# Performance work log

Measured on AMD Instinct MI355X. Metric: run time of the kernel, lower is better.

## Reference

```python
import jax, jax.numpy as jnp
import numpy as np

TOP_K = 2

def setup_inputs() -> dict:
    key = jax.random.key(0)
    ks = jax.random.split(key, 5)
    N, D, E, H, O = 2048, 1024, 16, 2048, 1024
    s_in = 1.0 / np.sqrt(D)
    s_h = 1.0 / np.sqrt(H)
    return {
        "z": jax.random.normal(ks[0], (N, D), dtype=jnp.float32),
        "router_w": jax.random.normal(ks[1], (E, D), dtype=jnp.float32) * s_in,
        "router_b": jnp.zeros((E,), dtype=jnp.float32),
        "w1": jax.random.normal(ks[2], (E, H, D), dtype=jnp.float32) * s_in,
        "b1": jnp.zeros((E, H), dtype=jnp.float32),
        "w2": jax.random.normal(ks[3], (E, O, H), dtype=jnp.float32) * s_h,
        "b2": jnp.zeros((E, O), dtype=jnp.float32),
    }

def reference(z, router_w, router_b, w1, b1, w2, b2):
    # Router: softmax over experts, then top-k with renormalized weights
    logits = z @ router_w.T + router_b                      # [N, E]
    probs = jax.nn.softmax(logits, axis=-1)                 # [N, E]
    topk_prob, topk_idx = jax.lax.top_k(probs, TOP_K)       # [N, K]
    topk_prob = topk_prob / topk_prob.sum(axis=-1, keepdims=True)

    # Dense all-expert MLP (faithful to original mix(): every expert on every token)
    h = jax.nn.gelu(jnp.einsum('nd,ehd->neh', z, w1) + b1, approximate=False)  # [N, E, H]
    expert_out = jnp.einsum('neh,eoh->neo', h, w2) + b2                        # [N, E, O]

    # Gather top-k expert outputs and combine with routing weights
    picked = jnp.take_along_axis(expert_out, topk_idx[:, :, None], axis=1)     # [N, K, O]
    return (picked * topk_prob[:, :, None]).sum(axis=1)                        # [N, O]
```

## Files before the change

### kernel.cpp

```cpp
#include <hip/hip_runtime.h>
#include <hip/hip_bf16.h>
#include <math.h>

#define N_TOK 2048
#define DIM   1024
#define NE    16
#define NH    2048
#define NO    1024

typedef __attribute__((ext_vector_type(8))) short short8;
typedef __attribute__((ext_vector_type(4))) float f32x4;

__device__ __forceinline__ unsigned short f2bf(float f) {
  union { float f; unsigned u; } v; v.f = f;
  unsigned r = v.u + 0x7FFFu + ((v.u >> 16) & 1u);
  return (unsigned short)(r >> 16);
}

__device__ __forceinline__ short8 pack8(float4 a, float4 b) {
  short8 r;
  r[0] = (short)f2bf(a.x); r[1] = (short)f2bf(a.y);
  r[2] = (short)f2bf(a.z); r[3] = (short)f2bf(a.w);
  r[4] = (short)f2bf(b.x); r[5] = (short)f2bf(b.y);
  r[6] = (short)f2bf(b.z); r[7] = (short)f2bf(b.w);
  return r;
}

__device__ __forceinline__ unsigned pkbf(float x, float y) {
  float2 f; f.x = x; f.y = y;
  __hip_bfloat162 b = __float22bfloat162_rn(f);
  unsigned u; __builtin_memcpy(&u, &b, 4);
  return u;
}
__device__ __forceinline__ short8 cvt8(float4 a, float4 b) {
  union { short8 s; unsigned u[4]; } r;
  r.u[0] = pkbf(a.x, a.y); r.u[1] = pkbf(a.z, a.w);
  r.u[2] = pkbf(b.x, b.y); r.u[3] = pkbf(b.z, b.w);
  return r.s;
}

__device__ __forceinline__ void glds16(const void* g, void* l) {
  __builtin_amdgcn_global_load_lds(
      (const __attribute__((address_space(1))) void*)g,
      (__attribute__((address_space(3))) void*)l, 16, 0, 0);
}

__global__ __launch_bounds__(256) void router_kernel(
    const float* __restrict__ z, const float* __restrict__ rw,
    const float* __restrict__ rb, int* __restrict__ counts,
    int* __restrict__ list, float* __restrict__ tkw) {
  const int n = blockIdx.x;
  const int t = threadIdx.x;
  const int e = t >> 4, sub = t & 15;
  const float* zr = z + (size_t)n * DIM;
  const float* wr = rw + (size_t)e * DIM;
  double acc = 0.0;
#pragma unroll
  for (int i = 0; i < 16; ++i) {
    const int d = i * 64 + sub * 4;
    const float4 zv = *(const float4*)(zr + d);
    const float4 wv = *(const float4*)(wr + d);
    acc += (double)zv.x * wv.x + (double)zv.y * wv.y
         + (double)zv.z * wv.z + (double)zv.w * wv.w;
  }
  acc += __shfl_xor(acc, 8, 16);
  acc += __shfl_xor(acc, 4, 16);
  acc += __shfl_xor(acc, 2, 16);
  acc += __shfl_xor(acc, 1, 16);
  __shared__ double logits[NE];
  if (sub == 0) logits[e] = acc + (double)rb[e];
  __syncthreads();
  if (t == 0) {
    int i0 = -1, i1 = -1; double v0 = -1e300, v1 = -1e300;
    for (int i = 0; i < NE; ++i) {
      const double v = logits[i];
      if (v > v0) { v1 = v0; i1 = i0; v0 = v; i0 = i; }
      else if (v > v1) { v1 = v; i1 = i; }
    }
    const double w0 = 1.0 / (1.0 + exp(v1 - v0));
    tkw[n * 2 + 0] = (float)w0;
    tkw[n * 2 + 1] = (float)(1.0 - w0);
    const int p0 = atomicAdd(&counts[i0], 1); list[i0 * N_TOK + p0] = n * 2;
    const int p1 = atomicAdd(&counts[i1], 1); list[i1 * N_TOK + p1] = n * 2 + 1;
  }
}

__global__ __launch_bounds__(256) void convert_z_kernel(
    const float* __restrict__ z, unsigned short* __restrict__ zbf) {
  const int i = (blockIdx.x * 256 + threadIdx.x) * 8;
  const float4 a = *(const float4*)(z + i);
  const float4 b = *(const float4*)(z + i + 4);
  *(short8*)(zbf + i) = pack8(a, b);
}

#define BM 128
#define BN 128
#define BK 64
#define NNT1 (NH / BN)
#define NNT2 (NO / BN)
#define MT_LEVELS 8
#define NT1 (DIM / BK)
#define NT2 (NH / BK)
#define ASZ (BM * BK * 2)
#define BSZ (BN * BK * 2)

__device__ __forceinline__ void decode_bid(int bid, int nent, int& mt, int& ent) {
  if (bid < 2 * nent) {
    mt = (bid >> 3) & 1;
    ent = (bid >> 4) * 8 + (bid & 7);
  } else {
    const int t2 = bid - 2 * nent;
    mt = 2 + t2 / nent;
    ent = t2 - (mt - 2) * nent;
  }
}

__global__ __launch_bounds__(256, 2) void gemm1_kernel(
    const unsigned short* __restrict__ zbf, const float* __restrict__ w1,
    const float* __restrict__ b1, const int* __restrict__ counts,
    const int* __restrict__ list, unsigned short* __restrict__ h) {
  int mt, ent;
  decode_bid(blockIdx.x, NE * NNT1, mt, ent);
  const int e  = ent >> 4;
  const int nt = ent & 15;
  const int ne = counts[e];
  if (mt * BM >= ne) return;
  const int t = threadIdx.x;

  __shared__ __align__(16) unsigned char As[2 * ASZ];
  __shared__ __align__(16) unsigned char Bs[2 * BSZ];
  __shared__ int ent_s[BM];
  if (t < BM) {
    const int idx = mt * BM + t;
    ent_s[t] = (idx < ne) ? list[e * N_TOK + idx] : -1;
  }
  __syncthreads();

  const int lane = t & 63, w = t >> 6;
  const unsigned short* aP[4];
  unsigned char* aL[4];
  {
    const int l3 = lane >> 3, c7 = lane & 7;
#pragma unroll
    for (int p = 0; p < 4; ++p) {
      const int CI = w + 4 * p;
      const int R = 8 * CI + l3;
      const int c = c7 ^ (R & 7);
      const int en = ent_s[R];
      aP[p] = zbf + (size_t)(en >= 0 ? (en >> 1) : 0) * DIM + c * 8;
      aL[p] = As + CI * 1024;
    }
  }
  const int bR = w * 32 + (lane >> 1);
  const int bh = lane & 1;
  const float* bSrc = w1 + ((size_t)e * NH + (size_t)(nt * BN + bR)) * DIM + bh * 32;
  unsigned char* bW[4];
#pragma unroll
  for (int j = 0; j < 4; ++j)
    bW[j] = Bs + bR * 128 + (((bh * 4 + j) ^ (bR & 7)) << 4);

  const int wm = (w & 1) * 64, wn = (w >> 1) * 64;
  const int l15 = lane & 15, quad = lane >> 4;

  f32x4 acc[4][4];
#pragma unroll
  for (int i = 0; i < 4; ++i)
#pragma unroll
    for (int j = 0; j < 4; ++j) acc[i][j] = (f32x4){0.f, 0.f, 0.f, 0.f};

  float4 breg[8];
#pragma unroll
  for (int p = 0; p < 4; ++p) glds16(aP[p], aL[p]);
#pragma unroll
  for (int j = 0; j < 8; ++j) breg[j] = *(const float4*)(bSrc + j * 4);
#pragma unroll
  for (int j = 0; j < 4; ++j)
    *(short8*)(bW[j]) = cvt8(breg[2 * j], breg[2 * j + 1]);
  __syncthreads();

  for (int kt = 0; kt < NT1; ++kt) {
    const int cur = kt & 1, nxt = cur ^ 1;
    const int k1 = (kt + 1) * BK;
    if (kt + 1 < NT1) {
#pragma unroll
      for (int p = 0; p < 4; ++p) glds16(aP[p] + k1, aL[p] + nxt * ASZ);
#pragma unroll
      for (int j = 0; j < 8; ++j) breg[j] = *(const float4*)(bSrc + k1 + j * 4);
    }
    const unsigned char* Ac = As + cur * ASZ;
    const unsigned char* Bc = Bs + cur * BSZ;
#pragma unroll
    for (int kk = 0; kk < BK; kk += 32) {
      short8 af[4], bfr[4];
      const int c0 = (kk >> 3) + quad;
#pragma unroll
      for (int i = 0; i < 4; ++i) {
        const int R = wm + i * 16 + l15;
        af[i] = *(const short8*)(Ac + R * 128 + ((c0 ^ (R & 7)) << 4));
      }
#pragma unroll
      for (int j = 0; j < 4; ++j) {
        const int R = wn + j * 16 + l15;
        bfr[j] = *(const short8*)(Bc + R * 128 + ((c0 ^ (R & 7)) << 4));
      }
#pragma unroll
      for (int i = 0; i < 4; ++i)
#pragma unroll
        for (int j = 0; j < 4; ++j)
          acc[i][j] = __builtin_amdgcn_mfma_f32_16x16x32_bf16(af[i], bfr[j], acc[i][j], 0, 0, 0);
    }
    if (kt + 1 < NT1) {
#pragma unroll
      for (int j = 0; j < 4; ++j)
        *(short8*)(bW[j] + nxt * BSZ) = cvt8(breg[2 * j], breg[2 * j + 1]);
      __syncthreads();
    }
  }

  const int r4 = quad * 4;
#pragma unroll
  for (int i = 0; i < 4; ++i) {
#pragma unroll
    for (int reg = 0; reg < 4; ++reg) {
      const int row = wm + i * 16 + r4 + reg;
      const int en = ent_s[row];
      if (en < 0) continue;
      unsigned short* hrow = h + (size_t)en * NH;
#pragma unroll
      for (int j = 0; j < 4; ++j) {
        const int col = nt * BN + wn + j * 16 + l15;
        float v = acc[i][j][reg] + b1[e * NH + col];
        v = 0.5f * v * (1.0f + erff(v * 0.70710678118654752f));
        hrow[col] = f2bf(v);
      }
    }
  }
}

__global__ __launch_bounds__(256, 2) void gemm2_kernel(
    const unsigned short* __restrict__ h, const float* __restrict__ w2,
    const float* __restrict__ b2, const int* __restrict__ counts,
    const int* __restrict__ list, float* __restrict__ contrib) {
  int mt, ent;
  decode_bid(blockIdx.x, NE * NNT2, mt, ent);
  const int e  = ent >> 3;
  const int nt = ent & 7;
  const int ne = counts[e];
  if (mt * BM >= ne) return;
  const int t = threadIdx.x;

  __shared__ __align__(16) unsigned char As[2 * ASZ];
  __shared__ __align__(16) unsigned char Bs[2 * BSZ];
  __shared__ int ent_s[BM];
  if (t < BM) {
    const int idx = mt * BM + t;
    ent_s[t] = (idx < ne) ? list[e * N_TOK + idx] : -1;
  }
  __syncthreads();

  const int lane = t & 63, w = t >> 6;
  const unsigned short* aP[4];
  unsigned char* aL[4];
  {
    const int l3 = lane >> 3, c7 = lane & 7;
#pragma unroll
    for (int p = 0; p < 4; ++p) {
      const int CI = w + 4 * p;
      const int R = 8 * CI + l3;
      const int c = c7 ^ (R & 7);
      const int en = ent_s[R];
      aP[p] = h + (size_t)(en >= 0 ? en : 0) * NH + c * 8;
      aL[p] = As + CI * 1024;
    }
  }
  const int bR = w * 32 + (lane >> 1);
  const int bh = lane & 1;
  const float* bSrc = w2 + ((size_t)e * NO + (size_t)(nt * BN + bR)) * NH + bh * 32;
  unsigned char* bW[4];
#pragma unroll
  for (int j = 0; j < 4; ++j)
    bW[j] = Bs + bR * 128 + (((bh * 4 + j) ^ (bR & 7)) << 4);

  const int wm = (w & 1) * 64, wn = (w >> 1) * 64;
  const int l15 = lane & 15, quad = lane >> 4;

  f32x4 acc[4][4];
#pragma unroll
  for (int i = 0; i < 4; ++i)
#pragma unroll
    for (int j = 0; j < 4; ++j) acc[i][j] = (f32x4){0.f, 0.f, 0.f, 0.f};

  float4 breg[8];
#pragma unroll
  for (int p = 0; p < 4; ++p) glds16(aP[p], aL[p]);
#pragma unroll
  for (int j = 0; j < 8; ++j) breg[j] = *(const float4*)(bSrc + j * 4);
#pragma unroll
  for (int j = 0; j < 4; ++j)
    *(short8*)(bW[j]) = cvt8(breg[2 * j], breg[2 * j + 1]);
  __syncthreads();

  for (int kt = 0; kt < NT2; ++kt) {
    const int cur = kt & 1, nxt = cur ^ 1;
    const int k1 = (kt + 1) * BK;
    if (kt + 1 < NT2) {
#pragma unroll
      for (int p = 0; p < 4; ++p) glds16(aP[p] + k1, aL[p] + nxt * ASZ);
#pragma unroll
      for (int j = 0; j < 8; ++j) breg[j] = *(const float4*)(bSrc + k1 + j * 4);
    }
    const unsigned char* Ac = As + cur * ASZ;
    const unsigned char* Bc = Bs + cur * BSZ;
#pragma unroll
    for (int kk = 0; kk < BK; kk += 32) {
      short8 af[4], bfr[4];
      const int c0 = (kk >> 3) + quad;
#pragma unroll
      for (int i = 0; i < 4; ++i) {
        const int R = wm + i * 16 + l15;
        af[i] = *(const short8*)(Ac + R * 128 + ((c0 ^ (R & 7)) << 4));
      }
#pragma unroll
      for (int j = 0; j < 4; ++j) {
        const int R = wn + j * 16 + l15;
        bfr[j] = *(const short8*)(Bc + R * 128 + ((c0 ^ (R & 7)) << 4));
      }
#pragma unroll
      for (int i = 0; i < 4; ++i)
#pragma unroll
        for (int j = 0; j < 4; ++j)
          acc[i][j] = __builtin_amdgcn_mfma_f32_16x16x32_bf16(af[i], bfr[j], acc[i][j], 0, 0, 0);
    }
    if (kt + 1 < NT2) {
#pragma unroll
      for (int j = 0; j < 4; ++j)
        *(short8*)(bW[j] + nxt * BSZ) = cvt8(breg[2 * j], breg[2 * j + 1]);
      __syncthreads();
    }
  }

  const int r4 = quad * 4;
#pragma unroll
  for (int i = 0; i < 4; ++i) {
#pragma unroll
    for (int reg = 0; reg < 4; ++reg) {
      const int row = wm + i * 16 + r4 + reg;
      const int en = ent_s[row];
      if (en < 0) continue;
      float* crow = contrib + (size_t)en * NO;
#pragma unroll
      for (int j = 0; j < 4; ++j) {
        const int col = nt * BN + wn + j * 16 + l15;
        crow[col] = acc[i][j][reg] + b2[e * NO + col];
      }
    }
  }
}

__global__ __launch_bounds__(256) void combine_kernel(
    const float* __restrict__ contrib, const float* __restrict__ tkw,
    float* __restrict__ out) {
  const int gid = blockIdx.x * 256 + threadIdx.x;
  const int n = gid >> 8;
  const int c = (gid & 255) * 4;
  const float w0 = tkw[n * 2], w1 = tkw[n * 2 + 1];
  const float4 a = *(const float4*)(contrib + (size_t)(n * 2) * NO + c);
  const float4 b = *(const float4*)(contrib + (size_t)(n * 2 + 1) * NO + c);
  float4 o;
  o.x = w0 * a.x + w1 * b.x; o.y = w0 * a.y + w1 * b.y;
  o.z = w0 * a.z + w1 * b.z; o.w = w0 * a.w + w1 * b.w;
  *(float4*)(out + (size_t)n * NO + c) = o;
}

extern "C" void kernel_launch(void* const* d_in, const int* in_sizes, int n_in,
                              void* d_out, int out_size, void* d_ws, size_t ws_size,
                              hipStream_t stream) {
  const float* z  = (const float*)d_in[0];
  const float* rw = (const float*)d_in[1];
  const float* rb = (const float*)d_in[2];
  const float* w1 = (const float*)d_in[3];
  const float* b1 = (const float*)d_in[4];
  const float* w2 = (const float*)d_in[5];
  const float* b2 = (const float*)d_in[6];
  float* out = (float*)d_out;

  char* ws = (char*)d_ws;
  int*   counts = (int*)ws;
  int*   list   = (int*)(ws + 256);
  float* tkw    = (float*)(ws + 256 + 131072);
  unsigned short* zbf = (unsigned short*)(ws + 262144);
  unsigned short* h = (unsigned short*)(ws + 262144 + 4194304);
  float* contrib = (float*)(ws + 262144 + 4194304 + 16777216);

  hipMemsetAsync(counts, 0, NE * sizeof(int), stream);
  convert_z_kernel<<<(N_TOK * DIM / 8) / 256, 256, 0, stream>>>(z, zbf);
  router_kernel<<<N_TOK, 256, 0, stream>>>(z, rw, rb, counts, list, tkw);
  gemm1_kernel<<<MT_LEVELS * NE * NNT1, 256, 0, stream>>>(zbf, w1, b1, counts, list, h);
  gemm2_kernel<<<MT_LEVELS * NE * NNT2, 256, 0, stream>>>(h, w2, b2, counts, list, contrib);
  combine_kernel<<<(N_TOK * (NO / 4)) / 256, 256, 0, stream>>>(contrib, tkw, out);
}
```

Measured before the change: 500.6 us.

## Load expert weights straight into MFMA registers, bypass LDS, remap blocks per XCD

The B operand (fp32 expert weights) is now loaded by each lane directly in MFMA fragment layout and converted to bf16 in registers, so the B shared-memory staging and its write/read traffic go away. The weight loads are prefetched one K-step ahead, with explicit vmcnt waits and raw s_barrier replacing __syncthreads. Block IDs are remapped so consecutive blocks on an XCD share an expert, which should improve L2 reuse. GEMM2 uses a narrower 64-column tile and a higher occupancy bound to fill more CUs. Per-lane global loads are less coalesced (32-byte chunks per row), and the hand-set vmcnt counts are fragile.

```diff
diff --git a/kernel.cpp b/kernel.cpp
--- a/kernel.cpp
+++ b/kernel.cpp
@@ -94,41 +94,34 @@
 }
 
 #define BM 128
-#define BN 128
 #define BK 64
-#define NNT1 (NH / BN)
-#define NNT2 (NO / BN)
-#define MT_LEVELS 8
 #define NT1 (DIM / BK)
 #define NT2 (NH / BK)
 #define ASZ (BM * BK * 2)
-#define BSZ (BN * BK * 2)
-
-__device__ __forceinline__ void decode_bid(int bid, int nent, int& mt, int& ent) {
-  if (bid < 2 * nent) {
-    mt = (bid >> 3) & 1;
-    ent = (bid >> 4) * 8 + (bid & 7);
-  } else {
-    const int t2 = bid - 2 * nent;
-    mt = 2 + t2 / nent;
-    ent = t2 - (mt - 2) * nent;
-  }
+#define BN1 128
+#define BN2 64
+#define MT_LEVELS 8
+#define GRID_GEMM (MT_LEVELS * NE * 16)
+
+__device__ __forceinline__ void decode_bid_xcd(int bid, int& mt, int& e, int& nt) {
+  const int slot = bid >> 3;
+  mt = slot >> 5;
+  const int rem = slot & 31;
+  e = (bid & 7) + ((rem & 1) << 3);
+  nt = rem >> 1;
 }
 
 __global__ __launch_bounds__(256, 2) void gemm1_kernel(
     const unsigned short* __restrict__ zbf, const float* __restrict__ w1,
     const float* __restrict__ b1, const int* __restrict__ counts,
     const int* __restrict__ list, unsigned short* __restrict__ h) {
-  int mt, ent;
-  decode_bid(blockIdx.x, NE * NNT1, mt, ent);
-  const int e  = ent >> 4;
-  const int nt = ent & 15;
+  int mt, e, nt;
+  decode_bid_xcd(blockIdx.x, mt, e, nt);
   const int ne = counts[e];
   if (mt * BM >= ne) return;
   const int t = threadIdx.x;
 
   __shared__ __align__(16) unsigned char As[2 * ASZ];
-  __shared__ __align__(16) unsigned char Bs[2 * BSZ];
   __shared__ int ent_s[BM];
   if (t < BM) {
     const int idx = mt * BM + t;
@@ -151,69 +144,77 @@
       aL[p] = As + CI * 1024;
     }
   }
-  const int bR = w * 32 + (lane >> 1);
-  const int bh = lane & 1;
-  const float* bSrc = w1 + ((size_t)e * NH + (size_t)(nt * BN + bR)) * DIM + bh * 32;
-  unsigned char* bW[4];
-#pragma unroll
-  for (int j = 0; j < 4; ++j)
-    bW[j] = Bs + bR * 128 + (((bh * 4 + j) ^ (bR & 7)) << 4);
-
   const int wm = (w & 1) * 64, wn = (w >> 1) * 64;
   const int l15 = lane & 15, quad = lane >> 4;
 
+  const float* bRow[4];
+#pragma unroll
+  for (int j = 0; j < 4; ++j)
+    bRow[j] = w1 + ((size_t)e * NH + (size_t)(nt * BN1 + wn + j * 16 + l15)) * DIM + quad * 8;
+
   f32x4 acc[4][4];
 #pragma unroll
   for (int i = 0; i < 4; ++i)
 #pragma unroll
     for (int j = 0; j < 4; ++j) acc[i][j] = (f32x4){0.f, 0.f, 0.f, 0.f};
 
-  float4 breg[8];
+  float4 breg[16];
 #pragma unroll
   for (int p = 0; p < 4; ++p) glds16(aP[p], aL[p]);
-#pragma unroll
-  for (int j = 0; j < 8; ++j) breg[j] = *(const float4*)(bSrc + j * 4);
+  __builtin_amdgcn_sched_barrier(0);
 #pragma unroll
   for (int j = 0; j < 4; ++j)
-    *(short8*)(bW[j]) = cvt8(breg[2 * j], breg[2 * j + 1]);
-  __syncthreads();
-
+#pragma unroll
+    for (int s = 0; s < 2; ++s) {
+      breg[(j * 2 + s) * 2 + 0] = *(const float4*)(bRow[j] + s * 32);
+      breg[(j * 2 + s) * 2 + 1] = *(const float4*)(bRow[j] + s * 32 + 4);
+    }
+  __builtin_amdgcn_sched_barrier(0);
+  asm volatile("s_waitcnt vmcnt(16)" ::: "memory");
+  __builtin_amdgcn_s_barrier();
+
+#pragma unroll 2
   for (int kt = 0; kt < NT1; ++kt) {
     const int cur = kt & 1, nxt = cur ^ 1;
-    const int k1 = (kt + 1) * BK;
+    short8 bfr[2][4];
+#pragma unroll
+    for (int j = 0; j < 4; ++j)
+#pragma unroll
+      for (int s = 0; s < 2; ++s)
+        bfr[s][j] = cvt8(breg[(j * 2 + s) * 2 + 0], breg[(j * 2 + s) * 2 + 1]);
     if (kt + 1 < NT1) {
+      const int k1 = (kt + 1) * BK;
 #pragma unroll
       for (int p = 0; p < 4; ++p) glds16(aP[p] + k1, aL[p] + nxt * ASZ);
-#pragma unroll
-      for (int j = 0; j < 8; ++j) breg[j] = *(const float4*)(bSrc + k1 + j * 4);
+      __builtin_amdgcn_sched_barrier(0);
+#pragma unroll
+      for (int j = 0; j < 4; ++j)
+#pragma unroll
+        for (int s = 0; s < 2; ++s) {
+          breg[(j * 2 + s) * 2 + 0] = *(const float4*)(bRow[j] + k1 + s * 32);
+          breg[(j * 2 + s) * 2 + 1] = *(const float4*)(bRow[j] + k1 + s * 32 + 4);
+        }
+      __builtin_amdgcn_sched_barrier(0);
     }
     const unsigned char* Ac = As + cur * ASZ;
-    const unsigned char* Bc = Bs + cur * BSZ;
-#pragma unroll
-    for (int kk = 0; kk < BK; kk += 32) {
-      short8 af[4], bfr[4];
-      const int c0 = (kk >> 3) + quad;
+#pragma unroll
+    for (int s = 0; s < 2; ++s) {
+      short8 af[4];
+      const int c0 = s * 4 + quad;
 #pragma unroll
       for (int i = 0; i < 4; ++i) {
         const int R = wm + i * 16 + l15;
         af[i] = *(const short8*)(Ac + R * 128 + ((c0 ^ (R & 7)) << 4));
       }
 #pragma unroll
-      for (int j = 0; j < 4; ++j) {
-        const int R = wn + j * 16 + l15;
-        bfr[j] = *(const short8*)(Bc + R * 128 + ((c0 ^ (R & 7)) << 4));
-      }
-#pragma unroll
       for (int i = 0; i < 4; ++i)
 #pragma unroll
         for (int j = 0; j < 4; ++j)
-          acc[i][j] = __builtin_amdgcn_mfma_f32_16x16x32_bf16(af[i], bfr[j], acc[i][j], 0, 0, 0);
+          acc[i][j] = __builtin_amdgcn_mfma_f32_16x16x32_bf16(af[i], bfr[s][j], acc[i][j], 0, 0, 0);
     }
     if (kt + 1 < NT1) {
-#pragma unroll
-      for (int j = 0; j < 4; ++j)
-        *(short8*)(bW[j] + nxt * BSZ) = cvt8(breg[2 * j], breg[2 * j + 1]);
-      __syncthreads();
+      asm volatile("s_waitcnt vmcnt(16)" ::: "memory");
+      __builtin_amdgcn_s_barrier();
     }
   }
 
@@ -228,7 +229,7 @@
       unsigned short* hrow = h + (size_t)en * NH;
 #pragma unroll
       for (int j = 0; j < 4; ++j) {
-        const int col = nt * BN + wn + j * 16 + l15;
+        const int col = nt * BN1 + wn + j * 16 + l15;
         float v = acc[i][j][reg] + b1[e * NH + col];
         v = 0.5f * v * (1.0f + erff(v * 0.70710678118654752f));
         hrow[col] = f2bf(v);
@@ -237,20 +238,17 @@
   }
 }
 
-__global__ __launch_bounds__(256, 2) void gemm2_kernel(
+__global__ __launch_bounds__(256, 3) void gemm2_kernel(
     const unsigned short* __restrict__ h, const float* __restrict__ w2,
     const float* __restrict__ b2, const int* __restrict__ counts,
     const int* __restrict__ list, float* __restrict__ contrib) {
-  int mt, ent;
-  decode_bid(blockIdx.x, NE * NNT2, mt, ent);
-  const int e  = ent >> 3;
-  const int nt = ent & 7;
+  int mt, e, nt;
+  decode_bid_xcd(blockIdx.x, mt, e, nt);
   const int ne = counts[e];
   if (mt * BM >= ne) return;
   const int t = threadIdx.x;
 
   __shared__ __align__(16) unsigned char As[2 * ASZ];
-  __shared__ __align__(16) unsigned char Bs[2 * BSZ];
   __shared__ int ent_s[BM];
   if (t < BM) {
     const int idx = mt * BM + t;
@@ -273,69 +271,77 @@
       aL[p] = As + CI * 1024;
     }
   }
-  const int bR = w * 32 + (lane >> 1);
-  const int bh = lane & 1;
-  const float* bSrc = w2 + ((size_t)e * NO + (size_t)(nt * BN + bR)) * NH + bh * 32;
-  unsigned char* bW[4];
-#pragma unroll
-  for (int j = 0; j < 4; ++j)
-    bW[j] = Bs + bR * 128 + (((bh * 4 + j) ^ (bR & 7)) << 4);
-
-  const int wm = (w & 1) * 64, wn = (w >> 1) * 64;
+  const int wm = (w & 1) * 64, wn = (w >> 1) * 32;
   const int l15 = lane & 15, quad = lane >> 4;
 
-  f32x4 acc[4][4];
+  const float* bRow[2];
+#pragma unroll
+  for (int j = 0; j < 2; ++j)
+    bRow[j] = w2 + ((size_t)e * NO + (size_t)(nt * BN2 + wn + j * 16 + l15)) * NH + quad * 8;
+
+  f32x4 acc[4][2];
 #pragma unroll
   for (int i = 0; i < 4; ++i)
 #pragma unroll
-    for (int j = 0; j < 4; ++j) acc[i][j] = (f32x4){0.f, 0.f, 0.f, 0.f};
+    for (int j = 0; j < 2; ++j) acc[i][j] = (f32x4){0.f, 0.f, 0.f, 0.f};
 
   float4 breg[8];
 #pragma unroll
   for (int p = 0; p < 4; ++p) glds16(aP[p], aL[p]);
-#pragma unroll
-  for (int j = 0; j < 8; ++j) breg[j] = *(const float4*)(bSrc + j * 4);
-#pragma unroll
-  for (int j = 0; j < 4; ++j)
-    *(short8*)(bW[j]) = cvt8(breg[2 * j], breg[2 * j + 1]);
-  __syncthreads();
-
+  __builtin_amdgcn_sched_barrier(0);
+#pragma unroll
+  for (int j = 0; j < 2; ++j)
+#pragma unroll
+    for (int s = 0; s < 2; ++s) {
+      breg[(j * 2 + s) * 2 + 0] = *(const float4*)(bRow[j] + s * 32);
+      breg[(j * 2 + s) * 2 + 1] = *(const float4*)(bRow[j] + s * 32 + 4);
+    }
+  __builtin_amdgcn_sched_barrier(0);
+  asm volatile("s_waitcnt vmcnt(8)" ::: "memory");
+  __builtin_amdgcn_s_barrier();
+
+#pragma unroll 2
   for (int kt = 0; kt < NT2; ++kt) {
     const int cur = kt & 1, nxt = cur ^ 1;
-    const int k1 = (kt + 1) * BK;
+    short8 bfr[2][2];
+#pragma unroll
+    for (int j = 0; j < 2; ++j)
+#pragma unroll
+      for (int s = 0; s < 2; ++s)
+        bfr[s][j] = cvt8(breg[(j * 2 + s) * 2 + 0], breg[(j * 2 + s) * 2 + 1]);
     if (kt + 1 < NT2) {
+      const int k1 = (kt + 1) * BK;
 #pragma unroll
       for (int p = 0; p < 4; ++p) glds16(aP[p] + k1, aL[p] + nxt * ASZ);
-#pragma unroll
-      for (int j = 0; j < 8; ++j) breg[j] = *(const float4*)(bSrc + k1 + j * 4);
+      __builtin_amdgcn_sched_barrier(0);
+#pragma unroll
+      for (int j = 0; j < 2; ++j)
+#pragma unroll
+        for (int s = 0; s < 2; ++s) {
+          breg[(j * 2 + s) * 2 + 0] = *(const float4*)(bRow[j] + k1 + s * 32);
+          breg[(j * 2 + s) * 2 + 1] = *(const float4*)(bRow[j] + k1 + s * 32 + 4);
+        }
+      __builtin_amdgcn_sched_barrier(0);
     }
     const unsigned char* Ac = As + cur * ASZ;
-    const unsigned char* Bc = Bs + cur * BSZ;
-#pragma unroll
-    for (int kk = 0; kk < BK; kk += 32) {
-      short8 af[4], bfr[4];
-      const int c0 = (kk >> 3) + quad;
+#pragma unroll
+    for (int s = 0; s < 2; ++s) {
+      short8 af[4];
+      const int c0 = s * 4 + quad;
 #pragma unroll
       for (int i = 0; i < 4; ++i) {
         const int R = wm + i * 16 + l15;
         af[i] = *(const short8*)(Ac + R * 128 + ((c0 ^ (R & 7)) << 4));
       }
 #pragma unroll
-      for (int j = 0; j < 4; ++j) {
-        const int R = wn + j * 16 + l15;
-        bfr[j] = *(const short8*)(Bc + R * 128 + ((c0 ^ (R & 7)) << 4));
-      }
-#pragma unroll
       for (int i = 0; i < 4; ++i)
 #pragma unroll
-        for (int j = 0; j < 4; ++j)
-          acc[i][j] = __builtin_amdgcn_mfma_f32_16x16x32_bf16(af[i], bfr[j], acc[i][j], 0, 0, 0);
+        for (int j = 0; j < 2; ++j)
+          acc[i][j] = __builtin_amdgcn_mfma_f32_16x16x32_bf16(af[i], bfr[s][j], acc[i][j], 0, 0, 0);
     }
     if (kt + 1 < NT2) {
-#pragma unroll
-      for (int j = 0; j < 4; ++j)
-        *(short8*)(bW[j] + nxt * BSZ) = cvt8(breg[2 * j], breg[2 * j + 1]);
-      __syncthreads();
+      asm volatile("s_waitcnt vmcnt(8)" ::: "memory");
+      __builtin_amdgcn_s_barrier();
     }
   }
 
@@ -349,8 +355,8 @@
       if (en < 0) continue;
       float* crow = contrib + (size_t)en * NO;
 #pragma unroll
-      for (int j = 0; j < 4; ++j) {
-        const int col = nt * BN + wn + j * 16 + l15;
+      for (int j = 0; j < 2; ++j) {
+        const int col = nt * BN2 + wn + j * 16 + l15;
         crow[col] = acc[i][j][reg] + b2[e * NO + col];
       }
     }
@@ -395,7 +401,7 @@
   hipMemsetAsync(counts, 0, NE * sizeof(int), stream);
   convert_z_kernel<<<(N_TOK * DIM / 8) / 256, 256, 0, stream>>>(z, zbf);
   router_kernel<<<N_TOK, 256, 0, stream>>>(z, rw, rb, counts, list, tkw);
-  gemm1_kernel<<<MT_LEVELS * NE * NNT1, 256, 0, stream>>>(zbf, w1, b1, counts, list, h);
-  gemm2_kernel<<<MT_LEVELS * NE * NNT2, 256, 0, stream>>>(h, w2, b2, counts, list, contrib);
+  gemm1_kernel<<<GRID_GEMM, 256, 0, stream>>>(zbf, w1, b1, counts, list, h);
+  gemm2_kernel<<<GRID_GEMM, 256, 0, stream>>>(h, w2, b2, counts, list, contrib);
   combine_kernel<<<(N_TOK * (NO / 4)) / 256, 256, 0, stream>>>(contrib, tkw, out);
 }
```

New measurement: 519.8 us. 3.8% more time.
